# Optimization experiments

Measured on AMD Instinct MI355X. Metric: run time of the kernel, lower is better.

Reference implementation:

```python
import jax, jax.numpy as jnp
import numpy as np

N_LEVELS = 16
N_FEATS = 2
LOG2_HASH = 19
HASHMAP_SIZE = 2 ** LOG2_HASH
BASE_RES = 16
FINEST_RES = 2048
PER_LEVEL_SCALE = np.exp((np.log(FINEST_RES) - np.log(BASE_RES)) / (N_LEVELS - 1))
PRIMES = np.array([1, 2654435761, 805459861], dtype=np.uint32)
# corner offsets in the order i(x), j(y), k(z) -> index i*4 + j*2 + k (matches torch loops)
CORNER_OFFSETS = np.array([[i, j, k] for i in range(2) for j in range(2) for k in range(2)], dtype=np.int32)
N_POINTS = 2097152


def setup_inputs() -> dict:
    key = jax.random.key(0)
    k_pos, k_emb = jax.random.split(key)
    positions = jax.random.uniform(k_pos, (N_POINTS, 3), dtype=jnp.float32)
    # hash tables init uniform(-1e-4, 1e-4), stacked across levels: [L, H, F]
    embeddings = jax.random.uniform(k_emb, (N_LEVELS, HASHMAP_SIZE, N_FEATS), dtype=jnp.float32,
                                    minval=-1e-4, maxval=1e-4)
    return {"positions": positions, "embeddings": embeddings}


def _encode_level(positions, table, level):
    res = int(np.floor(BASE_RES * PER_LEVEL_SCALE ** level))
    scaled = positions * res                      # [N,3]
    vmin = jnp.floor(scaled).astype(jnp.int32)    # [N,3], non-negative for positions in [0,1)
    w = scaled - vmin.astype(scaled.dtype)        # [N,3] trilinear weights
    corners = vmin[:, None, :] + CORNER_OFFSETS[None, :, :]  # [N,8,3]
    if (res + 1) ** 3 <= HASHMAP_SIZE:
        # dense voxel indexing
        r1 = res + 1
        idx = corners[..., 0] * (r1 * r1) + corners[..., 1] * r1 + corners[..., 2]
    else:
        # spatial hash: XOR of coord*prime; mod 2^19 == low 19 bits, so uint32
        # wraparound arithmetic reproduces torch's int64 math exactly.
        c = corners.astype(jnp.uint32)
        h = (c[..., 0] * PRIMES[0]) ^ (c[..., 1] * PRIMES[1]) ^ (c[..., 2] * PRIMES[2])
        idx = (h & jnp.uint32(HASHMAP_SIZE - 1)).astype(jnp.int32)
    idx = jnp.clip(idx, 0, HASHMAP_SIZE - 1)
    feats = table[idx]                             # [N,8,F] gather
    wx, wy, wz = w[:, 0:1], w[:, 1:2], w[:, 2:3]
    c00 = feats[:, 0] * (1 - wx) + feats[:, 4] * wx
    c01 = feats[:, 1] * (1 - wx) + feats[:, 5] * wx
    c10 = feats[:, 2] * (1 - wx) + feats[:, 6] * wx
    c11 = feats[:, 3] * (1 - wx) + feats[:, 7] * wx
    c0 = c00 * (1 - wy) + c10 * wy
    c1 = c01 * (1 - wy) + c11 * wy
    return c0 * (1 - wz) + c1 * wz                 # [N,F]


def reference(positions, embeddings):
    outs = [_encode_level(positions, embeddings[level], level) for level in range(N_LEVELS)]
    return jnp.concatenate(outs, axis=-1)          # [N, L*F]
```

## Files before the change

kernel.cpp:

```cpp
#include <hip/hip_runtime.h>
#include <cmath>

#define HE_N_LEVELS 16
#define HE_LOG2_HASH 19
#define HE_HASHMAP_SIZE (1u << HE_LOG2_HASH)
#define HE_HASH_MASK (HE_HASHMAP_SIZE - 1u)
#define HE_P1 2654435761u
#define HE_P2 805459861u

struct HEParams {
    int      res[HE_N_LEVELS];
    float    resf[HE_N_LEVELS];
    unsigned dense_bits;
};

__global__ __launch_bounds__(256) void he_encode_kernel(
    const float* __restrict__ pos,
    const float* __restrict__ emb,
    float* __restrict__ out,
    int n, HEParams prm)
{
    __shared__ float spos[256 * 3];
    const int tid   = threadIdx.x;
    const int bbase = blockIdx.x * 256;

    #pragma unroll
    for (int i = 0; i < 3; ++i) {
        const int g = bbase * 3 + tid + i * 256;
        if (g < n * 3) spos[tid + i * 256] = pos[g];
    }
    __syncthreads();

    const int p = bbase + tid;
    if (p >= n) return;

    const float x = spos[tid * 3 + 0];
    const float y = spos[tid * 3 + 1];
    const float z = spos[tid * 3 + 2];

    float outv[32];

    #pragma unroll
    for (int l = 0; l < HE_N_LEVELS; ++l) {
        const float rf = prm.resf[l];
        const float sx = x * rf, sy = y * rf, sz = z * rf;
        const float fx = floorf(sx), fy = floorf(sy), fz = floorf(sz);
        const float wx = sx - fx, wy = sy - fy, wz = sz - fz;
        const int vx = (int)fx, vy = (int)fy, vz = (int)fz;

        unsigned idx[8];
        if (prm.dense_bits & (1u << l)) {
            const int r1  = prm.res[l] + 1;
            const int r1s = r1 * r1;
            const int base = vx * r1s + vy * r1 + vz;
            idx[0] = base;             idx[1] = base + 1;
            idx[2] = base + r1;        idx[3] = base + r1 + 1;
            idx[4] = base + r1s;       idx[5] = base + r1s + 1;
            idx[6] = base + r1s + r1;  idx[7] = base + r1s + r1 + 1;
        } else {
            const unsigned hx0 = (unsigned)vx,        hx1 = hx0 + 1u;
            const unsigned hy0 = (unsigned)vy * HE_P1, hy1 = hy0 + HE_P1;
            const unsigned hz0 = (unsigned)vz * HE_P2, hz1 = hz0 + HE_P2;
            const unsigned t00 = hy0 ^ hz0, t01 = hy0 ^ hz1;
            const unsigned t10 = hy1 ^ hz0, t11 = hy1 ^ hz1;
            idx[0] = (hx0 ^ t00) & HE_HASH_MASK;
            idx[1] = (hx0 ^ t01) & HE_HASH_MASK;
            idx[2] = (hx0 ^ t10) & HE_HASH_MASK;
            idx[3] = (hx0 ^ t11) & HE_HASH_MASK;
            idx[4] = (hx1 ^ t00) & HE_HASH_MASK;
            idx[5] = (hx1 ^ t01) & HE_HASH_MASK;
            idx[6] = (hx1 ^ t10) & HE_HASH_MASK;
            idx[7] = (hx1 ^ t11) & HE_HASH_MASK;
        }

        const float2* __restrict__ tab =
            (const float2*)emb + (size_t)l * HE_HASHMAP_SIZE;

        const float2 f000 = tab[idx[0]];
        const float2 f001 = tab[idx[1]];
        const float2 f010 = tab[idx[2]];
        const float2 f011 = tab[idx[3]];
        const float2 f100 = tab[idx[4]];
        const float2 f101 = tab[idx[5]];
        const float2 f110 = tab[idx[6]];
        const float2 f111 = tab[idx[7]];

        const float omx = 1.f - wx, omy = 1.f - wy, omz = 1.f - wz;

        const float c00a = f000.x * omx + f100.x * wx;
        const float c00b = f000.y * omx + f100.y * wx;
        const float c01a = f001.x * omx + f101.x * wx;
        const float c01b = f001.y * omx + f101.y * wx;
        const float c10a = f010.x * omx + f110.x * wx;
        const float c10b = f010.y * omx + f110.y * wx;
        const float c11a = f011.x * omx + f111.x * wx;
        const float c11b = f011.y * omx + f111.y * wx;

        const float c0a = c00a * omy + c10a * wy;
        const float c0b = c00b * omy + c10b * wy;
        const float c1a = c01a * omy + c11a * wy;
        const float c1b = c01b * omy + c11b * wy;

        outv[2 * l]     = c0a * omz + c1a * wz;
        outv[2 * l + 1] = c0b * omz + c1b * wz;
    }

    float4* __restrict__ o4 = (float4*)(out + (size_t)p * 32);
    #pragma unroll
    for (int i = 0; i < 8; ++i)
        o4[i] = make_float4(outv[4 * i + 0], outv[4 * i + 1],
                            outv[4 * i + 2], outv[4 * i + 3]);
}

extern "C" void kernel_launch(void* const* d_in, const int* in_sizes, int n_in,
                              void* d_out, int out_size, void* d_ws, size_t ws_size,
                              hipStream_t stream) {
    const float* pos = (const float*)d_in[0];
    const float* emb = (const float*)d_in[1];
    float*       out = (float*)d_out;
    const int n = in_sizes[0] / 3;

    HEParams prm;
    const double scale = std::exp((std::log(2048.0) - std::log(16.0)) / 15.0);
    prm.dense_bits = 0u;
    for (int l = 0; l < HE_N_LEVELS; ++l) {
        const int r = (int)std::floor(16.0 * std::pow(scale, (double)l));
        prm.res[l]  = r;
        prm.resf[l] = (float)r;
        const long long r1 = (long long)r + 1;
        if (r1 * r1 * r1 <= (long long)HE_HASHMAP_SIZE) prm.dense_bits |= (1u << l);
    }

    const int nblocks = (n + 255) / 256;
    hipLaunchKernelGGL(he_encode_kernel, dim3(nblocks), dim3(256), 0, stream,
                       pos, emb, out, n, prm);
}
```

Before: 1.604 ms.

## Split encoding into per-level hash kernels with staged workspace and transpose

```diff
diff --git a/kernel.cpp b/kernel.cpp
--- a/kernel.cpp
+++ b/kernel.cpp
@@ -1,115 +1,151 @@
 #include <hip/hip_runtime.h>
 #include <cmath>
 
-#define HE_N_LEVELS 16
-#define HE_LOG2_HASH 19
-#define HE_HASHMAP_SIZE (1u << HE_LOG2_HASH)
-#define HE_HASH_MASK (HE_HASHMAP_SIZE - 1u)
-#define HE_P1 2654435761u
-#define HE_P2 805459861u
+#define NLV 16
+#define LOG2_HASH 19
+#define HSZ (1u << LOG2_HASH)
+#define HMASK (HSZ - 1u)
+#define HP1 2654435761u
+#define HP2 805459861u
+
+typedef float f2v __attribute__((ext_vector_type(2)));
+typedef float f4v __attribute__((ext_vector_type(4)));
 
 struct HEParams {
-    int      res[HE_N_LEVELS];
-    float    resf[HE_N_LEVELS];
-    unsigned dense_bits;
+    int   res[NLV];
+    float resf[NLV];
 };
 
-__global__ __launch_bounds__(256) void he_encode_kernel(
-    const float* __restrict__ pos,
-    const float* __restrict__ emb,
-    float* __restrict__ out,
+template<bool STAGED>
+__global__ __launch_bounds__(256) void he_dense(
+    const float* __restrict__ pos, const float* __restrict__ emb,
+    float* __restrict__ dst,
     int n, HEParams prm)
 {
     __shared__ float spos[256 * 3];
-    const int tid   = threadIdx.x;
+    const int tid = threadIdx.x;
     const int bbase = blockIdx.x * 256;
-
     #pragma unroll
     for (int i = 0; i < 3; ++i) {
         const int g = bbase * 3 + tid + i * 256;
-        if (g < n * 3) spos[tid + i * 256] = pos[g];
+        if (g < n * 3) spos[tid + i * 256] = __builtin_nontemporal_load(pos + g);
     }
     __syncthreads();
-
     const int p = bbase + tid;
     if (p >= n) return;
-
     const float x = spos[tid * 3 + 0];
     const float y = spos[tid * 3 + 1];
     const float z = spos[tid * 3 + 2];
 
-    float outv[32];
-
     #pragma unroll
-    for (int l = 0; l < HE_N_LEVELS; ++l) {
+    for (int l = 0; l < 5; ++l) {
         const float rf = prm.resf[l];
         const float sx = x * rf, sy = y * rf, sz = z * rf;
         const float fx = floorf(sx), fy = floorf(sy), fz = floorf(sz);
         const float wx = sx - fx, wy = sy - fy, wz = sz - fz;
-        const int vx = (int)fx, vy = (int)fy, vz = (int)fz;
+        const int r1 = prm.res[l] + 1, r1s = r1 * r1;
+        const int base = (int)fx * r1s + (int)fy * r1 + (int)fz;
 
-        unsigned idx[8];
-        if (prm.dense_bits & (1u << l)) {
-            const int r1  = prm.res[l] + 1;
-            const int r1s = r1 * r1;
-            const int base = vx * r1s + vy * r1 + vz;
-            idx[0] = base;             idx[1] = base + 1;
-            idx[2] = base + r1;        idx[3] = base + r1 + 1;
-            idx[4] = base + r1s;       idx[5] = base + r1s + 1;
-            idx[6] = base + r1s + r1;  idx[7] = base + r1s + r1 + 1;
-        } else {
-            const unsigned hx0 = (unsigned)vx,        hx1 = hx0 + 1u;
-            const unsigned hy0 = (unsigned)vy * HE_P1, hy1 = hy0 + HE_P1;
-            const unsigned hz0 = (unsigned)vz * HE_P2, hz1 = hz0 + HE_P2;
-            const unsigned t00 = hy0 ^ hz0, t01 = hy0 ^ hz1;
-            const unsigned t10 = hy1 ^ hz0, t11 = hy1 ^ hz1;
-            idx[0] = (hx0 ^ t00) & HE_HASH_MASK;
-            idx[1] = (hx0 ^ t01) & HE_HASH_MASK;
-            idx[2] = (hx0 ^ t10) & HE_HASH_MASK;
-            idx[3] = (hx0 ^ t11) & HE_HASH_MASK;
-            idx[4] = (hx1 ^ t00) & HE_HASH_MASK;
-            idx[5] = (hx1 ^ t01) & HE_HASH_MASK;
-            idx[6] = (hx1 ^ t10) & HE_HASH_MASK;
-            idx[7] = (hx1 ^ t11) & HE_HASH_MASK;
-        }
-
-        const float2* __restrict__ tab =
-            (const float2*)emb + (size_t)l * HE_HASHMAP_SIZE;
-
-        const float2 f000 = tab[idx[0]];
-        const float2 f001 = tab[idx[1]];
-        const float2 f010 = tab[idx[2]];
-        const float2 f011 = tab[idx[3]];
-        const float2 f100 = tab[idx[4]];
-        const float2 f101 = tab[idx[5]];
-        const float2 f110 = tab[idx[6]];
-        const float2 f111 = tab[idx[7]];
+        const f2v* __restrict__ tab = (const f2v*)(emb + (size_t)l * HSZ * 2);
+        const f2v f000 = tab[base];
+        const f2v f001 = tab[base + 1];
+        const f2v f010 = tab[base + r1];
+        const f2v f011 = tab[base + r1 + 1];
+        const f2v f100 = tab[base + r1s];
+        const f2v f101 = tab[base + r1s + 1];
+        const f2v f110 = tab[base + r1s + r1];
+        const f2v f111 = tab[base + r1s + r1 + 1];
 
         const float omx = 1.f - wx, omy = 1.f - wy, omz = 1.f - wz;
+        const f2v c00 = f000 * omx + f100 * wx;
+        const f2v c01 = f001 * omx + f101 * wx;
+        const f2v c10 = f010 * omx + f110 * wx;
+        const f2v c11 = f011 * omx + f111 * wx;
+        const f2v c0 = c00 * omy + c10 * wy;
+        const f2v c1 = c01 * omy + c11 * wy;
+        const f2v r  = c0 * omz + c1 * wz;
 
-        const float c00a = f000.x * omx + f100.x * wx;
-        const float c00b = f000.y * omx + f100.y * wx;
-        const float c01a = f001.x * omx + f101.x * wx;
-        const float c01b = f001.y * omx + f101.y * wx;
-        const float c10a = f010.x * omx + f110.x * wx;
-        const float c10b = f010.y * omx + f110.y * wx;
-        const float c11a = f011.x * omx + f111.x * wx;
-        const float c11b = f011.y * omx + f111.y * wx;
+        if (STAGED) {
+            __builtin_nontemporal_store(r, (f2v*)dst + (size_t)l * n + p);
+        } else {
+            *(f2v*)(dst + (size_t)p * 32 + 2 * l) = r;
+        }
+    }
+}
 
-        const float c0a = c00a * omy + c10a * wy;
-        const float c0b = c00b * omy + c10b * wy;
-        const float c1a = c01a * omy + c11a * wy;
-        const float c1b = c01b * omy + c11b * wy;
+template<bool STAGED>
+__global__ __launch_bounds__(256) void he_hash(
+    const float* __restrict__ pos,
+    const float* __restrict__ tab_,
+    float* __restrict__ dstl,
+    int n, float rf)
+{
+    __shared__ float spos[256 * 3];
+    const int tid = threadIdx.x;
+    const int bbase = blockIdx.x * 256;
+    #pragma unroll
+    for (int i = 0; i < 3; ++i) {
+        const int g = bbase * 3 + tid + i * 256;
+        if (g < n * 3) spos[tid + i * 256] = __builtin_nontemporal_load(pos + g);
+    }
+    __syncthreads();
+    const int p = bbase + tid;
+    if (p >= n) return;
+    const float x = spos[tid * 3 + 0];
+    const float y = spos[tid * 3 + 1];
+    const float z = spos[tid * 3 + 2];
 
-        outv[2 * l]     = c0a * omz + c1a * wz;
-        outv[2 * l + 1] = c0b * omz + c1b * wz;
+    const float sx = x * rf, sy = y * rf, sz = z * rf;
+    const float fx = floorf(sx), fy = floorf(sy), fz = floorf(sz);
+    const float wx = sx - fx, wy = sy - fy, wz = sz - fz;
+
+    const unsigned hx0 = (unsigned)(int)fx,        hx1 = hx0 + 1u;
+    const unsigned hy0 = (unsigned)(int)fy * HP1,  hy1 = hy0 + HP1;
+    const unsigned hz0 = (unsigned)(int)fz * HP2,  hz1 = hz0 + HP2;
+    const unsigned t00 = hy0 ^ hz0, t01 = hy0 ^ hz1;
+    const unsigned t10 = hy1 ^ hz0, t11 = hy1 ^ hz1;
+
+    const f2v* __restrict__ tab = (const f2v*)tab_;
+    const f2v f000 = tab[(hx0 ^ t00) & HMASK];
+    const f2v f001 = tab[(hx0 ^ t01) & HMASK];
+    const f2v f010 = tab[(hx0 ^ t10) & HMASK];
+    const f2v f011 = tab[(hx0 ^ t11) & HMASK];
+    const f2v f100 = tab[(hx1 ^ t00) & HMASK];
+    const f2v f101 = tab[(hx1 ^ t01) & HMASK];
+    const f2v f110 = tab[(hx1 ^ t10) & HMASK];
+    const f2v f111 = tab[(hx1 ^ t11) & HMASK];
+
+    const float omx = 1.f - wx, omy = 1.f - wy, omz = 1.f - wz;
+    const f2v c00 = f000 * omx + f100 * wx;
+    const f2v c01 = f001 * omx + f101 * wx;
+    const f2v c10 = f010 * omx + f110 * wx;
+    const f2v c11 = f011 * omx + f111 * wx;
+    const f2v c0 = c00 * omy + c10 * wy;
+    const f2v c1 = c01 * omy + c11 * wy;
+    const f2v r  = c0 * omz + c1 * wz;
+
+    if (STAGED) {
+        __builtin_nontemporal_store(r, (f2v*)dstl + p);
+    } else {
+        *(f2v*)(dstl + (size_t)p * 32) = r;
     }
+}
 
-    float4* __restrict__ o4 = (float4*)(out + (size_t)p * 32);
+__global__ __launch_bounds__(256) void he_tr(
+    const float* __restrict__ ws, float* __restrict__ out, int n)
+{
+    const int p = blockIdx.x * 256 + threadIdx.x;
+    if (p >= n) return;
+    f2v v[NLV];
     #pragma unroll
-    for (int i = 0; i < 8; ++i)
-        o4[i] = make_float4(outv[4 * i + 0], outv[4 * i + 1],
-                            outv[4 * i + 2], outv[4 * i + 3]);
+    for (int l = 0; l < NLV; ++l)
+        v[l] = __builtin_nontemporal_load((const f2v*)ws + (size_t)l * n + p);
+    f4v* __restrict__ o4 = (f4v*)(out + (size_t)p * 32);
+    #pragma unroll
+    for (int i = 0; i < 8; ++i) {
+        f4v o; o.x = v[2*i].x; o.y = v[2*i].y; o.z = v[2*i+1].x; o.w = v[2*i+1].y;
+        __builtin_nontemporal_store(o, o4 + i);
+    }
 }
 
 extern "C" void kernel_launch(void* const* d_in, const int* in_sizes, int n_in,
@@ -118,20 +154,34 @@
     const float* pos = (const float*)d_in[0];
     const float* emb = (const float*)d_in[1];
     float*       out = (float*)d_out;
+    float*       ws  = (float*)d_ws;
     const int n = in_sizes[0] / 3;
 
     HEParams prm;
     const double scale = std::exp((std::log(2048.0) - std::log(16.0)) / 15.0);
-    prm.dense_bits = 0u;
-    for (int l = 0; l < HE_N_LEVELS; ++l) {
+    for (int l = 0; l < NLV; ++l) {
         const int r = (int)std::floor(16.0 * std::pow(scale, (double)l));
         prm.res[l]  = r;
         prm.resf[l] = (float)r;
-        const long long r1 = (long long)r + 1;
-        if (r1 * r1 * r1 <= (long long)HE_HASHMAP_SIZE) prm.dense_bits |= (1u << l);
     }
 
-    const int nblocks = (n + 255) / 256;
-    hipLaunchKernelGGL(he_encode_kernel, dim3(nblocks), dim3(256), 0, stream,
-                       pos, emb, out, n, prm);
+    const int nb = (n + 255) / 256;
+    const bool staged = ws_size >= (size_t)NLV * n * 2 * sizeof(float);
+
+    if (staged) {
+        hipLaunchKernelGGL(he_dense<true>, dim3(nb), dim3(256), 0, stream,
+                           pos, emb, ws, n, prm);
+        for (int l = 5; l < NLV; ++l)
+            hipLaunchKernelGGL(he_hash<true>, dim3(nb), dim3(256), 0, stream,
+                               pos, emb + (size_t)l * HSZ * 2,
+                               ws + (size_t)l * n * 2, n, prm.resf[l]);
+        hipLaunchKernelGGL(he_tr, dim3(nb), dim3(256), 0, stream, ws, out, n);
+    } else {
+        hipLaunchKernelGGL(he_dense<false>, dim3(nb), dim3(256), 0, stream,
+                           pos, emb, out, n, prm);
+        for (int l = 5; l < NLV; ++l)
+            hipLaunchKernelGGL(he_hash<false>, dim3(nb), dim3(256), 0, stream,
+                               pos, emb + (size_t)l * HSZ * 2,
+                               out + 2 * l, n, prm.resf[l]);
+    }
 }
```

Measured after the change: 1.854 ms. +15.6%, slower.
